# Optimization experiments

Measured on AMD Instinct MI355X. Metric: run time of the kernel, lower is better.

## Reference

```python
import jax, jax.numpy as jnp
import numpy as np

ALPHA = 0.2  # LeakyReLU negative slope


def setup_inputs() -> dict:
    key = jax.random.key(0)
    ks = jax.random.split(key, 7)
    N, D, O, R = 50000, 128, 128, 64
    E1, E2 = 800000, 200000
    return {
        "input": jax.random.normal(ks[0], (N, D), jnp.float32),
        "edge": jax.random.randint(ks[1], (2, E1), 0, N),
        "edge_embed": jax.random.normal(ks[2], (E1, R), jnp.float32),
        "edge_list_nhop": jax.random.randint(ks[3], (2, E2), 0, N),
        "edge_embed_nhop": jax.random.normal(ks[4], (E2, R), jnp.float32),
        "a": jax.random.normal(ks[5], (O, 2 * D + R), jnp.float32) * 0.05,
        "a_2": jax.random.normal(ks[6], (1, O), jnp.float32) * 0.05,
    }


def _gat_forward(x, edge, e_embed, a, a_2):
    N, D = x.shape
    src, dst = edge[0], edge[1]
    # a @ [x_src; x_dst; e_embed]^T computed blockwise (avoids [E, 2D+R] concat)
    a_src, a_dst, a_rel = a[:, :D], a[:, D:2 * D], a[:, 2 * D:]
    edge_m = x[src] @ a_src.T + x[dst] @ a_dst.T + e_embed @ a_rel.T  # [E, O] == edge_m^T
    score = edge_m @ a_2[0]                                            # [E]
    powers = -jnp.where(score > 0, score, ALPHA * score)               # -LeakyReLU
    edge_e = jnp.exp(powers)                                           # [E]
    e_rowsum = jax.ops.segment_sum(edge_e, src, num_segments=N)[:, None]  # [N, 1]
    e_rowsum = jnp.where(e_rowsum == 0.0, 1e-12, e_rowsum)
    edge_w = edge_e[:, None] * edge_m                                  # [E, O]
    h_prime = jax.ops.segment_sum(edge_w, src, num_segments=N)         # [N, O]
    h_prime = h_prime / e_rowsum
    return jax.nn.elu(h_prime)  # concat=True path


def reference(input, edge, edge_embed, edge_list_nhop, edge_embed_nhop, a, a_2):
    edge_all = jnp.concatenate([edge, edge_list_nhop], axis=1)        # [2, E1+E2]
    embed_all = jnp.concatenate([edge_embed, edge_embed_nhop], axis=0)  # [E1+E2, R]
    return _gat_forward(input, edge_all, embed_all, a, a_2)
```

## Files before the change

kernel.cpp:

```cpp
#include <hip/hip_runtime.h>
#include <hip/hip_bf16.h>

#define LRELU_ALPHA 0.2f

typedef __bf16 bf16x8 __attribute__((ext_vector_type(8)));
typedef __bf16 bf16x4 __attribute__((ext_vector_type(4)));
typedef float f32x4 __attribute__((ext_vector_type(4)));

__global__ void k_prep_count(const float* __restrict__ a, const float* __restrict__ a2,
                             float* __restrict__ vall, __hip_bfloat16* __restrict__ ABf,
                             const int* __restrict__ e1, int E1,
                             const int* __restrict__ e2, int E2, int* __restrict__ cnt) {
    int idx = blockIdx.x * 256 + threadIdx.x;
    if (idx < 128 * 320) ABf[idx] = __float2bfloat16(a[idx]);
    if (idx < 320) {
        float s = 0.f;
#pragma unroll 8
        for (int o = 0; o < 128; ++o) s += a[o * 320 + idx] * a2[o];
        vall[idx] = s;
    }
    if (idx < E1 + E2) {
        int src = (idx < E1) ? e1[idx] : e2[idx - E1];
        atomicAdd(&cnt[src], 1);
    }
}

__global__ void k_node_scores(const float* __restrict__ x, const float* __restrict__ vall,
                              float* __restrict__ s_src, float* __restrict__ s_dst,
                              __hip_bfloat16* __restrict__ XBf, int N) {
    int wid = (int)((blockIdx.x * (size_t)blockDim.x + threadIdx.x) >> 6);
    int lane = threadIdx.x & 63;
    if (wid * 2 >= N) return;
    int half = lane >> 5;
    int j = lane & 31;
    int n = wid * 2 + half;
    int nc = (n < N) ? n : N - 1;
    f32x4 xv = *reinterpret_cast<const f32x4*>(x + (size_t)nc * 128 + 4 * j);
    if (n < N) {
        bf16x4 xb;
#pragma unroll
        for (int k = 0; k < 4; ++k) xb[k] = (__bf16)xv[k];
        *reinterpret_cast<bf16x4*>(XBf + (size_t)n * 128 + 4 * j) = xb;
    }
    f32x4 vs = *reinterpret_cast<const f32x4*>(vall + 4 * j);
    f32x4 vd = *reinterpret_cast<const f32x4*>(vall + 128 + 4 * j);
    float ps = xv.x * vs.x + xv.y * vs.y + xv.z * vs.z + xv.w * vs.w;
    float pd = xv.x * vd.x + xv.y * vd.y + xv.z * vd.z + xv.w * vd.w;
#pragma unroll
    for (int off = 1; off <= 16; off <<= 1) {
        ps += __shfl_xor(ps, off, 64);
        pd += __shfl_xor(pd, off, 64);
    }
    if (j == 0 && n < N) { s_src[n] = ps; s_dst[n] = pd; }
}

__global__ void k_scan1(const int* __restrict__ cnt, int* __restrict__ bsum, int N) {
    __shared__ int red[256];
    int t = threadIdx.x;
    int idx = blockIdx.x * 256 + t;
    red[t] = (idx < N) ? cnt[idx] : 0;
    __syncthreads();
    for (int off = 128; off > 0; off >>= 1) {
        if (t < off) red[t] += red[t + off];
        __syncthreads();
    }
    if (t == 0) bsum[blockIdx.x] = red[0];
}

__global__ void k_scan2(int* __restrict__ bsum, int nb) {
    __shared__ int tmp[256];
    int t = threadIdx.x;
    int v = (t < nb) ? bsum[t] : 0;
    tmp[t] = v;
    __syncthreads();
    for (int off = 1; off < 256; off <<= 1) {
        int add = (t >= off) ? tmp[t - off] : 0;
        __syncthreads();
        tmp[t] += add;
        __syncthreads();
    }
    if (t < nb) bsum[t] = tmp[t] - v;
}

__global__ void k_scan3(const int* __restrict__ cnt, const int* __restrict__ bsum,
                        int* __restrict__ start, int* __restrict__ cursor, int N, int E) {
    __shared__ int tmp[256];
    int t = threadIdx.x;
    int idx = blockIdx.x * 256 + t;
    int v = (idx < N) ? cnt[idx] : 0;
    tmp[t] = v;
    __syncthreads();
    for (int off = 1; off < 256; off <<= 1) {
        int add = (t >= off) ? tmp[t - off] : 0;
        __syncthreads();
        tmp[t] += add;
        __syncthreads();
    }
    if (idx < N) {
        int excl = tmp[t] - v + bsum[blockIdx.x];
        start[idx] = excl;
        cursor[idx] = excl;
    }
    if (blockIdx.x == 0 && t == 0) start[N] = E;
}

__global__ void k_scatter(const int* __restrict__ e1, int E1, const int* __restrict__ e2, int E2,
                          int* __restrict__ cursor, int2* __restrict__ se) {
    int e = blockIdx.x * blockDim.x + threadIdx.x;
    if (e >= E1 + E2) return;
    int src, dst;
    if (e < E1) { src = e1[e]; dst = e1[E1 + e]; }
    else { int t = e - E1; src = e2[t]; dst = e2[E2 + t]; }
    int p = atomicAdd(&cursor[src], 1);
    se[p] = make_int2(dst, e);
}

__global__ void k_gather(const __hip_bfloat16* __restrict__ XBf,
                         const float* __restrict__ emb1, const float* __restrict__ emb2, int E1,
                         const int* __restrict__ start, const int2* __restrict__ se,
                         const float* __restrict__ vall,
                         const float* __restrict__ s_src, const float* __restrict__ s_dst,
                         __hip_bfloat16* __restrict__ G, float* __restrict__ sxf, int N) {
    int n = (int)((blockIdx.x * (size_t)blockDim.x + threadIdx.x) >> 6);
    int lane = threadIdx.x & 63;
    if (n >= N) return;
    n = __builtin_amdgcn_readfirstlane(n);
    int g = lane >> 4;
    int t = lane & 15;
    int b = start[n], en = start[n + 1];
    float ssrc = s_src[n];
    f32x4 r4 = *reinterpret_cast<const f32x4*>(vall + 256 + 4 * t);
    f32x4 w4 = {0.f, 0.f, 0.f, 0.f};
    float u8[8] = {0.f, 0.f, 0.f, 0.f, 0.f, 0.f, 0.f, 0.f};
    float rs = 0.f;

    for (int p = b; p < en; p += 8) {
        int q0 = p + g;
        int q1 = p + 4 + g;
        int c0 = (q0 < en) ? q0 : en - 1;
        int c1 = (q1 < en) ? q1 : en - 1;
        int2 d0 = se[c0];
        int2 d1 = se[c1];
        const float* ep0 = (d0.y < E1) ? emb1 + (size_t)d0.y * 64 : emb2 + (size_t)(d0.y - E1) * 64;
        const float* ep1 = (d1.y < E1) ? emb1 + (size_t)d1.y * 64 : emb2 + (size_t)(d1.y - E1) * 64;
        f32x4 em0 = *reinterpret_cast<const f32x4*>(ep0 + 4 * t);
        f32x4 em1 = *reinterpret_cast<const f32x4*>(ep1 + 4 * t);
        bf16x8 xv0 = *reinterpret_cast<const bf16x8*>(XBf + (size_t)d0.x * 128 + 8 * t);
        bf16x8 xv1 = *reinterpret_cast<const bf16x8*>(XBf + (size_t)d1.x * 128 + 8 * t);
        float sd0 = s_dst[d0.x], sd1 = s_dst[d1.x];
        float t0 = em0.x * r4.x + em0.y * r4.y + em0.z * r4.z + em0.w * r4.w;
        float t1 = em1.x * r4.x + em1.y * r4.y + em1.z * r4.z + em1.w * r4.w;
#pragma unroll
        for (int off = 1; off <= 8; off <<= 1) {
            t0 += __shfl_xor(t0, off, 64);
            t1 += __shfl_xor(t1, off, 64);
        }
        float sc0 = ssrc + sd0 + t0;
        float sc1 = ssrc + sd1 + t1;
        float pz0 = sc0 > 0.f ? sc0 : LRELU_ALPHA * sc0;
        float pz1 = sc1 > 0.f ? sc1 : LRELU_ALPHA * sc1;
        float e0 = __expf(-pz0);
        float e1v = __expf(-pz1);
        if (q0 >= en) e0 = 0.f;
        if (q1 >= en) e1v = 0.f;
        rs += e0 + e1v;
        w4 += e0 * em0 + e1v * em1;
#pragma unroll
        for (int j = 0; j < 8; ++j)
            u8[j] += e0 * (float)xv0[j] + e1v * (float)xv1[j];
    }

#pragma unroll
    for (int j = 0; j < 8; ++j) {
        u8[j] += __shfl_xor(u8[j], 16, 64);
        u8[j] += __shfl_xor(u8[j], 32, 64);
    }
#pragma unroll
    for (int j = 0; j < 4; ++j) {
        w4[j] += __shfl_xor(w4[j], 16, 64);
        w4[j] += __shfl_xor(w4[j], 32, 64);
    }
    rs += __shfl_xor(rs, 16, 64);
    rs += __shfl_xor(rs, 32, 64);

    float inv = (rs == 0.f) ? 0.f : 1.f / rs;
    if (lane < 16) {
        __hip_bfloat16* gp = G + (size_t)n * 192;
        bf16x8 uu;
#pragma unroll
        for (int j = 0; j < 8; ++j) uu[j] = (__bf16)(u8[j] * inv);
        *reinterpret_cast<bf16x8*>(gp + 8 * lane) = uu;
        bf16x4 ww;
#pragma unroll
        for (int j = 0; j < 4; ++j) ww[j] = (__bf16)(w4[j] * inv);
        *reinterpret_cast<bf16x4*>(gp + 128 + 4 * lane) = ww;
        if (lane == 0) sxf[n] = (rs == 0.f) ? 0.f : 1.f;
    }
}

__global__ __launch_bounds__(256) void k_mfma(
    const __hip_bfloat16* __restrict__ XBf, const __hip_bfloat16* __restrict__ G,
    const __hip_bfloat16* __restrict__ ABf, const float* __restrict__ sxf,
    float* __restrict__ out, int N) {
    int lane = threadIdx.x & 63;
    int wave = threadIdx.x >> 6;
    int m0 = blockIdx.x * 64 + wave * 16;
    int q = lane >> 4, m = lane & 15;
    int rowm = m0 + m; if (rowm >= N) rowm = N - 1;
    const __hip_bfloat16* xr = XBf + (size_t)rowm * 128 + q * 8;
    const __hip_bfloat16* gr = G + (size_t)rowm * 192 + q * 8;
    const __hip_bfloat16* br = ABf + (size_t)m * 320 + q * 8;
    f32x4 acc[8];
#pragma unroll
    for (int c = 0; c < 8; ++c) acc[c] = f32x4{0.f, 0.f, 0.f, 0.f};

#pragma unroll
    for (int s = 0; s < 4; ++s) {
        bf16x8 af = *reinterpret_cast<const bf16x8*>(xr + s * 32);
#pragma unroll
        for (int c = 0; c < 8; ++c) {
            bf16x8 bf = *reinterpret_cast<const bf16x8*>(br + (size_t)c * 16 * 320 + s * 32);
            acc[c] = __builtin_amdgcn_mfma_f32_16x16x32_bf16(af, bf, acc[c], 0, 0, 0);
        }
    }
#pragma unroll
    for (int s = 0; s < 6; ++s) {
        bf16x8 af = *reinterpret_cast<const bf16x8*>(gr + s * 32);
#pragma unroll
        for (int c = 0; c < 8; ++c) {
            bf16x8 bf = *reinterpret_cast<const bf16x8*>(br + (size_t)c * 16 * 320 + 128 + s * 32);
            acc[c] = __builtin_amdgcn_mfma_f32_16x16x32_bf16(af, bf, acc[c], 0, 0, 0);
        }
    }

    float sxr[4];
#pragma unroll
    for (int r = 0; r < 4; ++r) {
        int n = m0 + q * 4 + r;
        sxr[r] = (n < N) ? sxf[n] : 0.f;
    }
#pragma unroll
    for (int c = 0; c < 8; ++c) {
#pragma unroll
        for (int r = 0; r < 4; ++r) {
            int n = m0 + q * 4 + r;
            if (n < N) {
                float h = acc[c][r] * sxr[r];
                out[(size_t)n * 128 + c * 16 + m] = h > 0.f ? h : __expf(h) - 1.f;
            }
        }
    }
}

extern "C" void kernel_launch(void* const* d_in, const int* in_sizes, int n_in,
                              void* d_out, int out_size, void* d_ws, size_t ws_size,
                              hipStream_t stream) {
    const float* x    = (const float*)d_in[0];
    const int*   e1   = (const int*)d_in[1];
    const float* emb1 = (const float*)d_in[2];
    const int*   e2   = (const int*)d_in[3];
    const float* emb2 = (const float*)d_in[4];
    const float* a    = (const float*)d_in[5];
    const float* a2   = (const float*)d_in[6];
    float* out = (float*)d_out;

    const int N  = in_sizes[0] / 128;
    const int E1 = in_sizes[1] / 2;
    const int E2 = in_sizes[3] / 2;
    const int E  = E1 + E2;
    const int NB = (N + 255) / 256;

    float* ws    = (float*)d_ws;
    float* vall  = ws;
    __hip_bfloat16* ABf = (__hip_bfloat16*)(ws + 512);
    float* s_src = ws + 512 + 20480;
    float* s_dst = s_src + N;
    float* sxf   = s_dst + N;
    int*   cnt    = (int*)(sxf + N);
    int*   bsum   = cnt + N;
    int*   start  = bsum + 256;
    int*   cursor = start + N + 1;
    size_t so = (size_t)((char*)(cursor + N + 1) - (char*)d_ws);
    so = (so + 15) & ~(size_t)15;
    int2*  se = (int2*)((char*)d_ws + so);
    size_t xo = so + (size_t)E * sizeof(int2);
    xo = (xo + 15) & ~(size_t)15;
    __hip_bfloat16* XBf = (__hip_bfloat16*)((char*)d_ws + xo);
    size_t go = xo + (size_t)N * 128 * sizeof(__hip_bfloat16);
    go = (go + 15) & ~(size_t)15;
    __hip_bfloat16* G = (__hip_bfloat16*)((char*)d_ws + go);

    size_t needed = go + (size_t)N * 192 * sizeof(__hip_bfloat16);
    if (ws_size < needed) return;

    hipMemsetAsync(cnt, 0, (size_t)N * sizeof(int), stream);

    int gridPC = ((E > 128 * 320 ? E : 128 * 320) + 255) / 256;
    k_prep_count<<<gridPC, 256, 0, stream>>>(a, a2, vall, ABf, e1, E1, e2, E2, cnt);
    int W = (N + 1) / 2;
    k_node_scores<<<(W * 64 + 255) / 256, 256, 0, stream>>>(x, vall, s_src, s_dst, XBf, N);
    k_scan1<<<NB, 256, 0, stream>>>(cnt, bsum, N);
    k_scan2<<<1, 256, 0, stream>>>(bsum, NB);
    k_scan3<<<NB, 256, 0, stream>>>(cnt, bsum, start, cursor, N, E);
    k_scatter<<<(E + 255) / 256, 256, 0, stream>>>(e1, E1, e2, E2, cursor, se);
    k_gather<<<(N * 64 + 255) / 256, 256, 0, stream>>>(
        XBf, emb1, emb2, E1, start, se, vall, s_src, s_dst, G, sxf, N);
    k_mfma<<<(N + 63) / 64, 256, 0, stream>>>(XBf, G, ABf, sxf, out, N);
}
```

Baseline: 541.4 us.

## Pre-sort edge embeddings into CSR order as bf16 with precomputed relation scores

The scatter kernel now reads each edge's fp32 embedding sequentially, computes its relation-score dot product, and writes a bf16 copy into the source-sorted CSR slot along with the dst index and score. The gather kernel then streams contiguous bf16 embeddings instead of doing random fp32 gathers by original edge id, and no longer recomputes the dot product. In exchange it adds an extra write and read of an E×64 bf16 buffer plus a warp-per-4-edges scatter layout. Embedding precision in the weighted sum drops to bf16.

```diff
diff --git a/kernel.cpp b/kernel.cpp
--- a/kernel.cpp
+++ b/kernel.cpp
@@ -104,21 +104,42 @@
     if (blockIdx.x == 0 && t == 0) start[N] = E;
 }
 
-__global__ void k_scatter(const int* __restrict__ e1, int E1, const int* __restrict__ e2, int E2,
-                          int* __restrict__ cursor, int2* __restrict__ se) {
-    int e = blockIdx.x * blockDim.x + threadIdx.x;
-    if (e >= E1 + E2) return;
+__global__ void k_scatter_copy(const int* __restrict__ e1, int E1,
+                               const int* __restrict__ e2, int E2,
+                               int* __restrict__ cursor,
+                               const float* __restrict__ emb1, const float* __restrict__ emb2,
+                               const float* __restrict__ vall,
+                               int* __restrict__ sd, float* __restrict__ tS,
+                               __hip_bfloat16* __restrict__ embS) {
+    int wid = (int)((blockIdx.x * (size_t)blockDim.x + threadIdx.x) >> 6);
+    int lane = threadIdx.x & 63;
+    int g = lane >> 4, t = lane & 15;
+    int e = wid * 4 + g;
+    int E = E1 + E2;
+    if (e >= E) return;
     int src, dst;
-    if (e < E1) { src = e1[e]; dst = e1[E1 + e]; }
-    else { int t = e - E1; src = e2[t]; dst = e2[E2 + t]; }
-    int p = atomicAdd(&cursor[src], 1);
-    se[p] = make_int2(dst, e);
+    const float* ep;
+    if (e < E1) { src = e1[e]; dst = e1[E1 + e]; ep = emb1 + (size_t)e * 64; }
+    else { int q = e - E1; src = e2[q]; dst = e2[E2 + q]; ep = emb2 + (size_t)q * 64; }
+    f32x4 em = *reinterpret_cast<const f32x4*>(ep + 4 * t);
+    f32x4 r4 = *reinterpret_cast<const f32x4*>(vall + 256 + 4 * t);
+    float tv = em.x * r4.x + em.y * r4.y + em.z * r4.z + em.w * r4.w;
+#pragma unroll
+    for (int off = 1; off <= 8; off <<= 1) tv += __shfl_xor(tv, off, 64);
+    int p = 0;
+    if (t == 0) p = atomicAdd(&cursor[src], 1);
+    p = __shfl(p, g * 16, 64);
+    bf16x4 eb;
+#pragma unroll
+    for (int k = 0; k < 4; ++k) eb[k] = (__bf16)em[k];
+    *reinterpret_cast<bf16x4*>(embS + (size_t)p * 64 + 4 * t) = eb;
+    if (t == 0) { sd[p] = dst; tS[p] = tv; }
 }
 
 __global__ void k_gather(const __hip_bfloat16* __restrict__ XBf,
-                         const float* __restrict__ emb1, const float* __restrict__ emb2, int E1,
-                         const int* __restrict__ start, const int2* __restrict__ se,
-                         const float* __restrict__ vall,
+                         const __hip_bfloat16* __restrict__ embS,
+                         const float* __restrict__ tS, const int* __restrict__ sd,
+                         const int* __restrict__ start,
                          const float* __restrict__ s_src, const float* __restrict__ s_dst,
                          __hip_bfloat16* __restrict__ G, float* __restrict__ sxf, int N) {
     int n = (int)((blockIdx.x * (size_t)blockDim.x + threadIdx.x) >> 6);
@@ -129,7 +150,6 @@
     int t = lane & 15;
     int b = start[n], en = start[n + 1];
     float ssrc = s_src[n];
-    f32x4 r4 = *reinterpret_cast<const f32x4*>(vall + 256 + 4 * t);
     f32x4 w4 = {0.f, 0.f, 0.f, 0.f};
     float u8[8] = {0.f, 0.f, 0.f, 0.f, 0.f, 0.f, 0.f, 0.f};
     float rs = 0.f;
@@ -139,22 +159,13 @@
         int q1 = p + 4 + g;
         int c0 = (q0 < en) ? q0 : en - 1;
         int c1 = (q1 < en) ? q1 : en - 1;
-        int2 d0 = se[c0];
-        int2 d1 = se[c1];
-        const float* ep0 = (d0.y < E1) ? emb1 + (size_t)d0.y * 64 : emb2 + (size_t)(d0.y - E1) * 64;
-        const float* ep1 = (d1.y < E1) ? emb1 + (size_t)d1.y * 64 : emb2 + (size_t)(d1.y - E1) * 64;
-        f32x4 em0 = *reinterpret_cast<const f32x4*>(ep0 + 4 * t);
-        f32x4 em1 = *reinterpret_cast<const f32x4*>(ep1 + 4 * t);
-        bf16x8 xv0 = *reinterpret_cast<const bf16x8*>(XBf + (size_t)d0.x * 128 + 8 * t);
-        bf16x8 xv1 = *reinterpret_cast<const bf16x8*>(XBf + (size_t)d1.x * 128 + 8 * t);
-        float sd0 = s_dst[d0.x], sd1 = s_dst[d1.x];
-        float t0 = em0.x * r4.x + em0.y * r4.y + em0.z * r4.z + em0.w * r4.w;
-        float t1 = em1.x * r4.x + em1.y * r4.y + em1.z * r4.z + em1.w * r4.w;
-#pragma unroll
-        for (int off = 1; off <= 8; off <<= 1) {
-            t0 += __shfl_xor(t0, off, 64);
-            t1 += __shfl_xor(t1, off, 64);
-        }
+        int d0 = sd[c0], d1 = sd[c1];
+        float t0 = tS[c0], t1 = tS[c1];
+        bf16x4 ev0 = *reinterpret_cast<const bf16x4*>(embS + (size_t)c0 * 64 + 4 * t);
+        bf16x4 ev1 = *reinterpret_cast<const bf16x4*>(embS + (size_t)c1 * 64 + 4 * t);
+        bf16x8 xv0 = *reinterpret_cast<const bf16x8*>(XBf + (size_t)d0 * 128 + 8 * t);
+        bf16x8 xv1 = *reinterpret_cast<const bf16x8*>(XBf + (size_t)d1 * 128 + 8 * t);
+        float sd0 = s_dst[d0], sd1 = s_dst[d1];
         float sc0 = ssrc + sd0 + t0;
         float sc1 = ssrc + sd1 + t1;
         float pz0 = sc0 > 0.f ? sc0 : LRELU_ALPHA * sc0;
@@ -164,7 +175,9 @@
         if (q0 >= en) e0 = 0.f;
         if (q1 >= en) e1v = 0.f;
         rs += e0 + e1v;
-        w4 += e0 * em0 + e1v * em1;
+        f32x4 f0 = {(float)ev0[0], (float)ev0[1], (float)ev0[2], (float)ev0[3]};
+        f32x4 f1 = {(float)ev1[0], (float)ev1[1], (float)ev1[2], (float)ev1[3]};
+        w4 += e0 * f0 + e1v * f1;
 #pragma unroll
         for (int j = 0; j < 8; ++j)
             u8[j] += e0 * (float)xv0[j] + e1v * (float)xv1[j];
@@ -280,10 +293,12 @@
     int*   bsum   = cnt + N;
     int*   start  = bsum + 256;
     int*   cursor = start + N + 1;
-    size_t so = (size_t)((char*)(cursor + N + 1) - (char*)d_ws);
-    so = (so + 15) & ~(size_t)15;
-    int2*  se = (int2*)((char*)d_ws + so);
-    size_t xo = so + (size_t)E * sizeof(int2);
+    int*   sd     = cursor + N + 1;
+    float* tS     = (float*)(sd + E);
+    size_t so = (size_t)((char*)(tS + E) - (char*)d_ws);
+    so = (so + 127) & ~(size_t)127;
+    __hip_bfloat16* embS = (__hip_bfloat16*)((char*)d_ws + so);
+    size_t xo = so + (size_t)E * 64 * sizeof(__hip_bfloat16);
     xo = (xo + 15) & ~(size_t)15;
     __hip_bfloat16* XBf = (__hip_bfloat16*)((char*)d_ws + xo);
     size_t go = xo + (size_t)N * 128 * sizeof(__hip_bfloat16);
@@ -302,8 +317,10 @@
     k_scan1<<<NB, 256, 0, stream>>>(cnt, bsum, N);
     k_scan2<<<1, 256, 0, stream>>>(bsum, NB);
     k_scan3<<<NB, 256, 0, stream>>>(cnt, bsum, start, cursor, N, E);
-    k_scatter<<<(E + 255) / 256, 256, 0, stream>>>(e1, E1, e2, E2, cursor, se);
+    int Wsc = (E + 3) / 4;
+    k_scatter_copy<<<(Wsc * 64 + 255) / 256, 256, 0, stream>>>(
+        e1, E1, e2, E2, cursor, emb1, emb2, vall, sd, tS, embS);
     k_gather<<<(N * 64 + 255) / 256, 256, 0, stream>>>(
-        XBf, emb1, emb2, E1, start, se, vall, s_src, s_dst, G, sxf, N);
+        XBf, embS, tS, sd, start, s_src, s_dst, G, sxf, N);
     k_mfma<<<(N + 63) / 64, 256, 0, stream>>>(XBf, G, ABf, sxf, out, N);
 }
```

After: 537.2 us. Within noise of the previous version (-0.8%).
